# Performance work log

Hardware: AMD Instinct MI355X
Metric: run time of the kernel (lower is better)

## Reference

```python
import jax, jax.numpy as jnp
import numpy as np

B, S, E, H, L = 64, 256, 640, 512, 2  # batch, seq_len, input_size(=embed+sum_depth), rnn_size, num_layers
ZDIM = L * 2 * 2 * H  # ziphidden output dim = num_layers * num_dirs * (h|c) * H = 4096


def setup_inputs() -> dict:
    key = jax.random.key(0)
    ks = jax.random.split(key, 16)
    s = 0.05  # small init scale (~1/sqrt(H)) to avoid gate saturation
    f32 = jnp.float32
    inp = {
        "input": jax.random.normal(ks[0], (B, S, E), f32),
        "eps": jax.random.normal(ks[1], (B, ZDIM), f32),
        # layer 0 (input E), stacked over 2 directions [fwd, rev]
        "w_ih0": jax.random.normal(ks[2], (2, 4 * H, E), f32) * s,
        "w_hh0": jax.random.normal(ks[3], (2, 4 * H, H), f32) * s,
        "b_ih0": jax.random.normal(ks[4], (2, 4 * H), f32) * s,
        "b_hh0": jax.random.normal(ks[5], (2, 4 * H), f32) * s,
        # layer 1 (input 2H from bidirectional layer-0 output)
        "w_ih1": jax.random.normal(ks[6], (2, 4 * H, 2 * H), f32) * s,
        "w_hh1": jax.random.normal(ks[7], (2, 4 * H, H), f32) * s,
        "b_ih1": jax.random.normal(ks[8], (2, 4 * H), f32) * s,
        "b_hh1": jax.random.normal(ks[9], (2, 4 * H), f32) * s,
        # linear heads (layer_dim*2 -> layer_dim*2)
        "W_mu": jax.random.normal(ks[10], (ZDIM, ZDIM), f32) * 0.02,
        "b_mu": jax.random.normal(ks[11], (ZDIM,), f32) * 0.02,
        "W_var": jax.random.normal(ks[12], (ZDIM, ZDIM), f32) * 0.02,
        "b_var": jax.random.normal(ks[13], (ZDIM,), f32) * 0.02,
    }
    return inp


def _lstm_cell(x, h, c, wih, whh, b):
    # gates order i, f, g, o (PyTorch convention)
    g = x @ wih.T + h @ whh.T + b
    i, f, gg, o = jnp.split(g, 4, axis=-1)
    c2 = jax.nn.sigmoid(f) * c + jax.nn.sigmoid(i) * jnp.tanh(gg)
    h2 = jax.nn.sigmoid(o) * jnp.tanh(c2)
    return h2, c2


def reference(input, eps, w_ih0, w_hh0, b_ih0, b_hh0, w_ih1, w_hh1, b_ih1, b_hh1, W_mu, b_mu, W_var, b_var):
    # Module does input.view(seq_len, batch, embed) (a reshape, not transpose) then
    # steps the LSTM one timestep at a time for seq_len-1 steps. Since each call is
    # a length-1 sequence, both directions see the same single step independently.
    x_seq = input.reshape(S, B, E)[: S - 1]
    W_ih, W_hh = [w_ih0, w_ih1], [w_hh0, w_hh1]
    Bias = [b_ih0 + b_hh0, b_ih1 + b_hh1]

    h0 = jnp.zeros((2 * L, B, H), input.dtype)  # [l0f, l0r, l1f, l1r]
    c0 = jnp.zeros((2 * L, B, H), input.dtype)

    def step(carry, x):
        h, c = carry
        hs, cs = [], []
        inp_l = x
        for l in range(L):
            hf, cf = _lstm_cell(inp_l, h[2 * l], c[2 * l], W_ih[l][0], W_hh[l][0], Bias[l][0])
            hr, cr = _lstm_cell(inp_l, h[2 * l + 1], c[2 * l + 1], W_ih[l][1], W_hh[l][1], Bias[l][1])
            hs += [hf, hr]
            cs += [cf, cr]
            inp_l = jnp.concatenate([hf, hr], axis=-1)  # layer output feeds next layer
        return (jnp.stack(hs), jnp.stack(cs)), None

    (hF, cF), _ = jax.lax.scan(step, (h0, c0), x_seq)

    # ziphidden: cat(h, c, dim=2) -> transpose(0,1) -> view(B, -1)
    z = jnp.concatenate([hF, cF], axis=2)            # [2L, B, 2H]
    z = jnp.transpose(z, (1, 0, 2)).reshape(B, -1)   # [B, ZDIM]

    mu = z @ W_mu.T + b_mu
    logvar = z @ W_var.T + b_var
    # reparameterize (training mode) with externally supplied eps
    return mu + eps * jnp.exp(0.5 * logvar)
```

## Files before the change

kernel.cpp:

```cpp
#include <hip/hip_runtime.h>
#include <hip/hip_bf16.h>
#include <cstddef>
#include <cstdint>

#define B     64
#define S     256
#define E     640
#define H     512
#define TSTEPS (S - 1)
#define ZDIM  4096
#define KT    64
#define HS    (B * H)
#define CELL64 8192
#define NBUF  4

#define FSLOT(c, s) (((c) << 7) + ((s) << 2))

typedef __attribute__((ext_vector_type(8)))  __bf16 bf16x8;
typedef __attribute__((ext_vector_type(16))) float  f32x16;
typedef unsigned long long ull;

__device__ __forceinline__ float sigf(float x) { return 1.0f / (1.0f + __expf(-x)); }
__device__ __forceinline__ float tanhfast(float x) { return 1.0f - 2.0f / (__expf(2.0f * x) + 1.0f); }

__device__ __forceinline__ unsigned short f2bf(float f) {
    union { float f; unsigned u; } x; x.f = f;
    unsigned r = x.u + 0x7fffu + ((x.u >> 16) & 1u);
    return (unsigned short)(r >> 16);
}
__device__ __forceinline__ float bf2f(unsigned short u) {
    union { unsigned u; float f; } x; x.u = ((unsigned)u) << 16;
    return x.f;
}
__device__ __forceinline__ unsigned pk2(float a, float b) {
    return (unsigned)f2bf(a) | ((unsigned)f2bf(b) << 16);
}

#define HSTORE64(p, v) __hip_atomic_store((p), (v), __ATOMIC_RELAXED, __HIP_MEMORY_SCOPE_AGENT)
#define HSTORE32(p, v) __hip_atomic_store((p), (v), __ATOMIC_RELAXED, __HIP_MEMORY_SCOPE_AGENT)

__device__ __forceinline__ uint4 cld16(const void* p) {
    uint4 v;
    asm volatile("global_load_dwordx4 %0, %1, off sc0 sc1"
                 : "=v"(v) : "v"(p) : "memory");
    return v;
}
__device__ __forceinline__ unsigned ldf(const unsigned* p) {
    unsigned v;
    asm volatile("global_load_dword %0, %1, off sc0 sc1"
                 : "=v"(v) : "v"(p) : "memory");
    return v;
}
__device__ __forceinline__ void cwait0() {
    asm volatile("s_waitcnt vmcnt(0)" ::: "memory");
    __builtin_amdgcn_sched_barrier(0);
}
__device__ __forceinline__ void vmw16() {
    asm volatile("s_waitcnt vmcnt(16)" ::: "memory");
    __builtin_amdgcn_sched_barrier(0);
}
__device__ __forceinline__ bf16x8 u2b(uint4 u) {
    union { uint4 u; bf16x8 b; } x; x.u = u; return x.b;
}


__global__ __launch_bounds__(256) void conv_x_kernel(
    const float* __restrict__ in, unsigned short* __restrict__ out, int n8)
{
    int i = blockIdx.x * 256 + threadIdx.x;
    if (i >= n8) return;
    const float4* p = (const float4*)(in + (size_t)i * 8);
    float4 a = p[0], b = p[1];
    unsigned short* o = out + (size_t)i * 8;
    o[0] = f2bf(a.x); o[1] = f2bf(a.y); o[2] = f2bf(a.z); o[3] = f2bf(a.w);
    o[4] = f2bf(b.x); o[5] = f2bf(b.y); o[6] = f2bf(b.z); o[7] = f2bf(b.w);
}

__global__ __launch_bounds__(256) void repack_w_kernel(
    const float* __restrict__ in, unsigned short* __restrict__ out, int K)
{
    int kc = K / 8;
    int i = blockIdx.x * 256 + threadIdx.x;
    if (i >= 2 * 2048 * kc) return;
    int k8 = i % kc;
    int n  = (i / kc) & 2047;
    int d  = i / (kc * 2048);
    int srow = (n & 3) * 512 + (n >> 2);
    const float* src = in + ((size_t)d * 2048 + srow) * K + (size_t)k8 * 8;
    unsigned short* dst = out + ((size_t)d * 2048 + n) * K + (size_t)k8 * 8;
    #pragma unroll
    for (int q = 0; q < 8; ++q) dst[q] = f2bf(src[q]);
}

__global__ __launch_bounds__(256) void pack_bias_kernel(
    const float* __restrict__ bih, const float* __restrict__ bhh, float* __restrict__ out)
{
    int i = blockIdx.x * 256 + threadIdx.x;
    if (i >= 4096) return;
    int d = i >> 11, n = i & 2047;
    int s = d * 2048 + (n & 3) * 512 + (n >> 2);
    out[i] = bih[s] + bhh[s];
}

__global__ __launch_bounds__(256) void xproj_kernel(
    const unsigned short* __restrict__ xb,
    const unsigned short* __restrict__ w0p,
    unsigned short* __restrict__ xp)
{
    extern __shared__ __align__(16) char lds[];
    const int tid = threadIdx.x;
    const int l   = tid & 63;
    const int w   = tid >> 6;
    const int wm  = w & 1, wn = w >> 1;
    const int d   = blockIdx.x >> 5;
    const int n0  = (blockIdx.x & 31) * 64;

    for (int idx = tid; idx < 64 * 80; idx += 256) {
        int r = idx / 80, k8 = idx % 80;
        bf16x8 v = *(const bf16x8*)(w0p + ((size_t)d*2048 + n0 + r)*640 + (size_t)k8*8);
        int o = k8*16 + r*16; o -= (o >= 1280) ? 1280 : 0;
        *(bf16x8*)(lds + r*1280 + o) = v;
    }
    __syncthreads();

    const int lrow  = wn * 32 + (l & 31);
    const int khalf = l >> 5;
    const char* ldsrow = lds + (size_t)lrow * 1280;
    const int rot = lrow * 16 + khalf * 16;
    const int t0 = blockIdx.y * 64;
    const int t1 = (t0 + 64 < TSTEPS) ? (t0 + 64) : TSTEPS;

    for (int t = t0; t < t1; ++t) {
        f32x16 a0, a1;
#pragma unroll
        for (int r = 0; r < 16; ++r) { a0[r] = 0.f; a1[r] = 0.f; }
        const unsigned short* Ax = xb + ((size_t)t*B + wm*32 + (l & 31))*E + khalf*8;
#pragma unroll 8
        for (int k0 = 0; k0 < E; k0 += 16) {
            bf16x8 a = *(const bf16x8*)(Ax + k0);
            int o = k0*2 + rot; o -= (o >= 1280) ? 1280 : 0;
            bf16x8 b = *(const bf16x8*)(ldsrow + o);
            if ((k0 >> 4) & 1) a1 = __builtin_amdgcn_mfma_f32_32x32x16_bf16(a, b, a1, 0, 0, 0);
            else               a0 = __builtin_amdgcn_mfma_f32_32x32x16_bf16(a, b, a0, 0, 0, 0);
        }
        size_t base = ((((size_t)t*2 + d)*64 + (n0 >> 5) + wn)*2 + wm)*1024 + (size_t)l*16;
        unsigned short* dst = xp + base;
        uint4 o0, o1;
        o0.x = pk2(a0[0]+a1[0],  a0[1]+a1[1]);
        o0.y = pk2(a0[2]+a1[2],  a0[3]+a1[3]);
        o0.z = pk2(a0[4]+a1[4],  a0[5]+a1[5]);
        o0.w = pk2(a0[6]+a1[6],  a0[7]+a1[7]);
        o1.x = pk2(a0[8]+a1[8],  a0[9]+a1[9]);
        o1.y = pk2(a0[10]+a1[10], a0[11]+a1[11]);
        o1.z = pk2(a0[12]+a1[12], a0[13]+a1[13]);
        o1.w = pk2(a0[14]+a1[14], a0[15]+a1[15]);
        *(uint4*)dst       = o0;
        *(uint4*)(dst + 8) = o1;
    }
}

__device__ __forceinline__ void poll_l0(const unsigned* flags, int d,
                                        unsigned traw, unsigned twar, int l)
{
    const unsigned* pd = flags + FSLOT(d, l & 31);
    const unsigned* pw = flags + FSLOT((l < 32) ? 2 : 3, l & 31);
    for (;;) {
        unsigned a = ldf(pd);
        unsigned b = ldf(pw);
        cwait0();
        if (__all((int)(a >= traw && b >= twar))) break;
        __builtin_amdgcn_s_sleep(1);
    }
}
__device__ __forceinline__ void poll_l1(const unsigned* flags, int d,
                                        unsigned k, int l)
{
    const unsigned* po = flags + FSLOT(2 + d, l & 31);
    const unsigned* pc = flags + FSLOT((l < 32) ? 0 : 1, l & 31);
    const unsigned town = k - 1u;
    for (;;) {
        unsigned a = ldf(po);
        unsigned b = ldf(pc);
        cwait0();
        if (__all((int)(a >= town && b >= k))) break;
        __builtin_amdgcn_s_sleep(1);
    }
}

__device__ __forceinline__ void hcell_c_lds(const void* hp, const char* ldsrow,
    int rotofs, int wrapB, f32x16& a0, f32x16& a1)
{
    uint4 hv[32];
#pragma unroll
    for (int m = 0; m < 32; ++m)
        hv[m] = cld16((const char*)hp + (size_t)m * 1024);
    cwait0();
#pragma unroll
    for (int m = 0; m < 32; ++m) {
        int o = m*32 + rotofs; o -= (o >= wrapB) ? wrapB : 0;
        bf16x8 b = *(const bf16x8*)(ldsrow + o);
        bf16x8 a = u2b(hv[m]);
        if (m & 1) a1 = __builtin_amdgcn_mfma_f32_32x32x16_bf16(a, b, a1, 0, 0, 0);
        else       a0 = __builtin_amdgcn_mfma_f32_32x32x16_bf16(a, b, a0, 0, 0, 0);
    }
}

__device__ __forceinline__ void issue16(uint4* hv, const char* hpB, int mb) {
#pragma unroll
    for (int j = 0; j < 16; ++j)
        hv[j] = cld16(hpB + (size_t)(mb + j) * 1024);
}
__device__ __forceinline__ void consume16_reg(const uint4* hv, const bf16x8* wf,
                                              int mb, f32x16& a0, f32x16& a1)
{
#pragma unroll
    for (int j = 0; j < 16; ++j) {
        const int m = mb + j;
        bf16x8 a = u2b(hv[j]);
        if (m & 1) a1 = __builtin_amdgcn_mfma_f32_32x32x16_bf16(a, wf[m], a1, 0, 0, 0);
        else       a0 = __builtin_amdgcn_mfma_f32_32x32x16_bf16(a, wf[m], a0, 0, 0, 0);
    }
}
__device__ __forceinline__ void consume16_lds(const uint4* hv, const char* ldsrow,
                                              int rotofs, int mb, f32x16& a0, f32x16& a1)
{
#pragma unroll
    for (int j = 0; j < 16; ++j) {
        const int m = mb + j;
        int o = (m*32 + rotofs) & 2047;
        bf16x8 b = *(const bf16x8*)(ldsrow + o);
        bf16x8 a = u2b(hv[j]);
        if (m & 1) a1 = __builtin_amdgcn_mfma_f32_32x32x16_bf16(a, b, a1, 0, 0, 0);
        else       a0 = __builtin_amdgcn_mfma_f32_32x32x16_bf16(a, b, a0, 0, 0, 0);
    }
}

template<bool XADD>
__device__ __forceinline__ void act_store(
    const f32x16& a0, const f32x16& a1, bf16x8 xpa, bf16x8 xpb,
    int unitg, int wm, int l, float* creg, float* hreg, ull* hq_cell)
{
    const int g  = l & 3;
    const int hi = l >> 5;
    union { bf16x8 v; unsigned short s[8]; } ua, ub;
    ua.v = xpa; ub.v = xpb;
    float gi[4], gf[4], gg[4], go[4];
#pragma unroll
    for (int r = 0; r < 16; ++r) {
        float v0 = a0[r] + a1[r];
        if (XADD) v0 += bf2f((r < 8) ? ua.s[r] : ub.s[r - 8]);
        float v1 = __shfl_xor(v0, 1);
        float v2 = __shfl_xor(v0, 2);
        float v3 = __shfl_xor(v0, 3);
        float pv[4] = {v0, v1, v2, v3};
        const int rg = r & 3, q = r >> 2;
        if (g == rg) { gi[q] = pv[rg^0]; gf[q] = pv[rg^1]; gg[q] = pv[rg^2]; go[q] = pv[rg^3]; }
    }
    const int ubase = unitg & ~3;
    ull* dst = hq_cell + wm*4096 + (ubase >> 4)*128 + ((ubase >> 3) & 1)*64
                       + ((ubase >> 2) & 1);
#pragma unroll
    for (int q = 0; q < 4; ++q) {
        int rl = g + 8*q + 4*hi;
        float cold = creg[q];
        float cnew = sigf(gf[q]) * cold + sigf(gi[q]) * tanhfast(gg[q]);
        float hnew = sigf(go[q]) * tanhfast(cnew);
        creg[q] = cnew;
        hreg[q] = hnew;
        unsigned m  = f2bf(hnew);
        unsigned o1 = __shfl_xor(m, 4);
        unsigned d0 = (unitg & 1) ? ((m << 16) | o1) : ((o1 << 16) | m);
        unsigned o2 = __shfl_xor(d0, 8);
        ull q64 = (unitg & 2) ? (((ull)d0 << 32) | (ull)o2) : (((ull)o2 << 32) | (ull)d0);
        if ((l & 12) == 0)
            HSTORE64(dst + rl*2, q64);
    }
}

template<int XPRE>
__global__ __launch_bounds__(256, 1) void persist_kernel(
    const unsigned short* __restrict__ xb,
    const unsigned short* __restrict__ w0p,
    const unsigned short* __restrict__ wh0p,
    const unsigned short* __restrict__ w1p,
    const unsigned short* __restrict__ wh1p,
    const float* __restrict__ b0p,
    const float* __restrict__ b1p,
    const unsigned short* __restrict__ xp,
    unsigned short* __restrict__ hbuf,
    float* __restrict__ cbuf,
    unsigned short* __restrict__ hplain,
    unsigned* __restrict__ flags)
{
    extern __shared__ __align__(16) char lds[];
    const int tid = threadIdx.x;
    const int l   = tid & 63;
    const int w   = tid >> 6;
    const int wm  = w & 1, wn = w >> 1;
    const int bid = blockIdx.x;
    const bool isL1 = bid >= 64;
    const int g2 = bid & 63;
    const int d  = g2 >> 5;
    const int n0 = (g2 & 31) * 64;
    const int myslot = g2 & 31;
    const int lrow  = wn * 32 + (l & 31);
    const int khalf = l >> 5;
    const int HHOFF = 64 * 1280;

    if (!isL1) {
        if (!XPRE) {
            for (int idx = tid; idx < 64 * 80; idx += 256) {
                int r = idx / 80, k8 = idx % 80;
                bf16x8 v = *(const bf16x8*)(w0p + ((size_t)d*2048 + n0 + r)*640 + (size_t)k8*8);
                int o = k8*16 + r*16; o -= (o >= 1280) ? 1280 : 0;
                *(bf16x8*)(lds + r*1280 + o) = v;
            }
        }
        const int hb0 = XPRE ? 0 : HHOFF;
        for (int idx = tid; idx < 64 * 64; idx += 256) {
            int r = idx / 64, k8 = idx % 64;
            bf16x8 v = *(const bf16x8*)(wh0p + ((size_t)d*2048 + n0 + r)*512 + (size_t)k8*8);
            int o = k8*16 + r*16; o -= (o >= 1024) ? 1024 : 0;
            *(bf16x8*)(lds + hb0 + r*1024 + o) = v;
        }
    } else {
        for (int idx = tid; idx < 64 * 128; idx += 256) {
            int r = idx / 128, k8 = idx % 128;
            bf16x8 v = *(const bf16x8*)(w1p + ((size_t)d*2048 + n0 + r)*1024 + (size_t)k8*8);
            int o = k8*16 + r*16; o -= (o >= 2048) ? 2048 : 0;
            *(bf16x8*)(lds + r*2048 + o) = v;
        }
    }
    __syncthreads();

    const float bias = (isL1 ? b1p : b0p)[d*2048 + n0 + lrow];
    const char* ldsrow_ih = lds + (size_t)lrow * (isL1 ? 2048 : 1280);
    const char* ldsrow_hh = lds + (XPRE ? 0 : HHOFF) + (size_t)lrow * 1024;
    const int rot = lrow * 16 + khalf * 16;
    const int unitg = ((n0 + lrow) >> 2);
    const int hoff  = wm*4096 + khalf*64 + (l & 31)*2;
    const int arow  = wm * 32 + (l & 31);
    float creg[4] = {0.f, 0.f, 0.f, 0.f};
    float hreg[4] = {0.f, 0.f, 0.f, 0.f};
    const ull* hb = (const ull*)hbuf;
    ull*       hw = (ull*)hbuf;
    const int mycell = isL1 ? (2 + d) : d;
    unsigned* myflag = flags + FSLOT(mycell, myslot);
    bf16x8 zero8 = {};

    bf16x8 wh[32];
    if (isL1) {
        const unsigned short* whl = wh1p + ((size_t)d*2048 + n0 + lrow)*512 + khalf*8;
#pragma unroll
        for (int m = 0; m < 32; ++m) wh[m] = *(const bf16x8*)(whl + m*16);
    }

    for (int k = 0; k <= TSTEPS; ++k) {
        const int rbuf = k % NBUF, wbuf = (k + 1) % NBUF;
        const size_t rb = (size_t)rbuf * 4 * CELL64;
        const size_t wb = (size_t)wbuf * 4 * CELL64;
        if (!isL1) {
            if (k < TSTEPS) {
                f32x16 a0, a1;
#pragma unroll
                for (int r = 0; r < 16; ++r) { a0[r] = bias; a1[r] = 0.f; }
                bf16x8 xpa = zero8, xpb = zero8;
                if (XPRE) {
                    size_t base = ((((size_t)k*2 + d)*64 + (n0 >> 5) + wn)*2 + wm)*1024
                                  + (size_t)l*16;
                    xpa = *(const bf16x8*)(xp + base);
                    xpb = *(const bf16x8*)(xp + base + 8);
                } else {
                    const unsigned short* Ax = xb + (size_t)k*B*E + (size_t)arow*E + khalf*8;
#pragma unroll 8
                    for (int k0 = 0; k0 < E; k0 += 16) {
                        bf16x8 a = *(const bf16x8*)(Ax + k0);
                        int o = k0*2 + rot; o -= (o >= 1280) ? 1280 : 0;
                        bf16x8 b = *(const bf16x8*)(ldsrow_ih + o);
                        if ((k0 >> 4) & 1) a1 = __builtin_amdgcn_mfma_f32_32x32x16_bf16(a, b, a1, 0, 0, 0);
                        else               a0 = __builtin_amdgcn_mfma_f32_32x32x16_bf16(a, b, a0, 0, 0, 0);
                    }
                }
                if (k >= 1) {
                    if (w == 0)
                        poll_l0(flags, d, (unsigned)k,
                                (k >= 3) ? (unsigned)(k - 3) : 0u, l);
                    __syncthreads();
                }
                hcell_c_lds((const char*)(hb + rb + (size_t)d*CELL64 + hoff),
                            ldsrow_hh, rot, 1024, a0, a1);
                act_store<true>(a0, a1, xpa, xpb, unitg, wm, l, creg, hreg,
                                hw + wb + (size_t)d*CELL64);
                asm volatile("s_waitcnt vmcnt(0)" ::: "memory");
                __syncthreads();
                if (tid == 0) HSTORE32(myflag, (unsigned)(k + 1));
            }
        } else {
            if (k >= 1) {
                f32x16 a0, a1;
#pragma unroll
                for (int r = 0; r < 16; ++r) { a0[r] = bias; a1[r] = 0.f; }
                if (w == 0) poll_l1(flags, d, (unsigned)k, l);
                __syncthreads();
                const char* hpO = (const char*)(hb + rb + (size_t)(2+d)*CELL64 + hoff);
                const char* hp0 = (const char*)(hb + rb + (size_t)0*CELL64 + hoff);
                const char* hp1 = (const char*)(hb + rb + (size_t)1*CELL64 + hoff);
                uint4 hvA[16], hvB[16];
                issue16(hvA, hpO, 0);
                issue16(hvB, hpO, 16);
                vmw16(); consume16_reg(hvA, wh, 0,  a0, a1);
                issue16(hvA, hp0, 0);
                vmw16(); consume16_reg(hvB, wh, 16, a0, a1);
                issue16(hvB, hp0, 16);
                vmw16(); consume16_lds(hvA, ldsrow_ih, rot, 0,  a0, a1);
                issue16(hvA, hp1, 0);
                vmw16(); consume16_lds(hvB, ldsrow_ih, rot, 16, a0, a1);
                issue16(hvB, hp1, 16);
                vmw16(); consume16_lds(hvA, ldsrow_ih, rot + 1024, 0,  a0, a1);
                cwait0(); consume16_lds(hvB, ldsrow_ih, rot + 1024, 16, a0, a1);
                act_store<false>(a0, a1, zero8, zero8, unitg, wm, l, creg, hreg,
                                 hw + wb + (size_t)(2+d)*CELL64);
                asm volatile("s_waitcnt vmcnt(0)" ::: "memory");
                __syncthreads();
                if (tid == 0) HSTORE32(myflag, (unsigned)k);
            }
        }
    }

    {
        float*          cc = cbuf   + (size_t)mycell * HS;
        unsigned short* hh = hplain + (size_t)mycell * HS;
        const int g = l & 3, hi = l >> 5;
#pragma unroll
        for (int q = 0; q < 4; ++q) {
            int row = 32*wm + g + 8*q + 4*hi;
            cc[(size_t)row * 512 + unitg] = creg[q];
            hh[(size_t)row * 512 + unitg] = f2bf(hreg[q]);
        }
    }
}

__global__ __launch_bounds__(256) void head_kernel(
    const unsigned short* __restrict__ hplain,
    const float* __restrict__ cbuf,
    const float* __restrict__ eps,
    const float* __restrict__ Wmu,  const float* __restrict__ bmu,
    const float* __restrict__ Wvar, const float* __restrict__ bvar,
    float* __restrict__ out)
{
    const int tid = threadIdx.x;
    const int b   = tid & 63;
    const int i   = blockIdx.x * 4 + (tid >> 6);

    __shared__ float zs[KT][B + 1];

    float amu = 0.f, alv = 0.f;
    const float* wm = Wmu  + (size_t)i * ZDIM;
    const float* wv = Wvar + (size_t)i * ZDIM;

    for (int k0 = 0; k0 < ZDIM; k0 += KT) {
        __syncthreads();
        for (int idx = tid; idx < (B * KT) / 4; idx += 256) {
            int bb  = idx / (KT / 4);
            int kq4 = (idx % (KT / 4)) * 4;
            int zk  = k0 + kq4;
            int cell = zk >> 10;
            int m    = zk & 1023;
            float4 v;
            if (m < H) {
                const unsigned short* hs = hplain + (size_t)cell * HS + (size_t)bb * H + m;
                v.x = bf2f(hs[0]); v.y = bf2f(hs[1]); v.z = bf2f(hs[2]); v.w = bf2f(hs[3]);
            } else {
                v = *(const float4*)(cbuf + (size_t)cell * HS + (size_t)bb * H + (m - H));
            }
            zs[kq4 + 0][bb] = v.x; zs[kq4 + 1][bb] = v.y;
            zs[kq4 + 2][bb] = v.z; zs[kq4 + 3][bb] = v.w;
        }
        __syncthreads();
        #pragma unroll
        for (int kk = 0; kk < KT; kk += 4) {
            float4 a = *(const float4*)(wm + k0 + kk);
            float4 c = *(const float4*)(wv + k0 + kk);
            float z0 = zs[kk + 0][b], z1 = zs[kk + 1][b];
            float z2 = zs[kk + 2][b], z3 = zs[kk + 3][b];
            amu += a.x * z0 + a.y * z1 + a.z * z2 + a.w * z3;
            alv += c.x * z0 + c.y * z1 + c.z * z2 + c.w * z3;
        }
    }
    float mu = amu + bmu[i];
    float lv = alv + bvar[i];
    out[(size_t)b * ZDIM + i] = mu + eps[(size_t)b * ZDIM + i] * __expf(0.5f * lv);
}

extern "C" void kernel_launch(void* const* d_in, const int* in_sizes, int n_in,
                              void* d_out, int out_size, void* d_ws, size_t ws_size,
                              hipStream_t stream) {
    const float* input = (const float*)d_in[0];
    const float* eps   = (const float*)d_in[1];
    const float* w_ih0 = (const float*)d_in[2];
    const float* w_hh0 = (const float*)d_in[3];
    const float* b_ih0 = (const float*)d_in[4];
    const float* b_hh0 = (const float*)d_in[5];
    const float* w_ih1 = (const float*)d_in[6];
    const float* w_hh1 = (const float*)d_in[7];
    const float* b_ih1 = (const float*)d_in[8];
    const float* b_hh1 = (const float*)d_in[9];
    const float* W_mu  = (const float*)d_in[10];
    const float* b_mu  = (const float*)d_in[11];
    const float* W_var = (const float*)d_in[12];
    const float* b_var = (const float*)d_in[13];
    float* out = (float*)d_out;

    uint8_t* base = (uint8_t*)d_ws;
    size_t off = 0;
    auto alloc = [&](size_t bytes) -> void* {
        void* p = base + off;
        off += (bytes + 255) & ~(size_t)255;
        return p;
    };
    unsigned short* xb   = (unsigned short*)alloc((size_t)TSTEPS * B * E * 2);
    unsigned short* w0p  = (unsigned short*)alloc((size_t)2 * 2048 * E * 2);
    unsigned short* wh0p = (unsigned short*)alloc((size_t)2 * 2048 * H * 2);
    unsigned short* w1p  = (unsigned short*)alloc((size_t)2 * 2048 * 1024 * 2);
    unsigned short* wh1p = (unsigned short*)alloc((size_t)2 * 2048 * H * 2);
    float* b0p = (float*)alloc(2 * 2048 * 4);
    float* b1p = (float*)alloc(2 * 2048 * 4);
    unsigned* flags      = (unsigned*)alloc(2048);
    unsigned short* hbuf = (unsigned short*)alloc((size_t)NBUF * 4 * HS * 2);
    float* cbuf          = (float*)alloc((size_t)4 * HS * 4);
    unsigned short* hplain = (unsigned short*)alloc((size_t)4 * HS * 2);
    unsigned short* xp   = (unsigned short*)alloc((size_t)TSTEPS * 2 * 2048 * B * 2);
    const bool XPRE = (ws_size >= off);

    hipMemsetAsync(flags, 0, 2048 + (size_t)NBUF * 4 * HS * 2, stream);

    conv_x_kernel<<<(TSTEPS * B * E / 8 + 255) / 256, 256, 0, stream>>>(input, xb, TSTEPS * B * E / 8);
    repack_w_kernel<<<(2 * 2048 * (E / 8) + 255) / 256, 256, 0, stream>>>(w_ih0, w0p, E);
    repack_w_kernel<<<(2 * 2048 * (H / 8) + 255) / 256, 256, 0, stream>>>(w_hh0, wh0p, H);
    repack_w_kernel<<<(2 * 2048 * (1024 / 8) + 255) / 256, 256, 0, stream>>>(w_ih1, w1p, 1024);
    repack_w_kernel<<<(2 * 2048 * (H / 8) + 255) / 256, 256, 0, stream>>>(w_hh1, wh1p, H);
    pack_bias_kernel<<<16, 256, 0, stream>>>(b_ih0, b_hh0, b0p);
    pack_bias_kernel<<<16, 256, 0, stream>>>(b_ih1, b_hh1, b1p);

    const size_t lds_persist = 144 * 1024;
    if (XPRE) {
        const size_t lds_xp = 84 * 1024;
        hipFuncSetAttribute((const void*)xproj_kernel,
                            hipFuncAttributeMaxDynamicSharedMemorySize, (int)lds_xp);
        xproj_kernel<<<dim3(64, 4), 256, lds_xp, stream>>>(xb, w0p, xp);
        hipFuncSetAttribute((const void*)persist_kernel<1>,
                            hipFuncAttributeMaxDynamicSharedMemorySize, (int)lds_persist);
        persist_kernel<1><<<128, 256, lds_persist, stream>>>(
            xb, w0p, wh0p, w1p, wh1p, b0p, b1p, xp, hbuf, cbuf, hplain, flags);
    } else {
        hipFuncSetAttribute((const void*)persist_kernel<0>,
                            hipFuncAttributeMaxDynamicSharedMemorySize, (int)lds_persist);
        persist_kernel<0><<<128, 256, lds_persist, stream>>>(
            xb, w0p, wh0p, w1p, wh1p, b0p, b1p, xp, hbuf, cbuf, hplain, flags);
    }

    head_kernel<<<ZDIM / 4, 256, 0, stream>>>(hplain, cbuf, eps, W_mu, b_mu, W_var, b_var, out);
}
```

Before: 2.922 ms.

## Fuse input projection into persistent kernel as producer blocks with flag sync

The separate xproj kernel and the fp32-to-bf16 conversion kernel are removed. The persistent kernel now launches 256 blocks, and the extra 128 blocks compute the layer-0 input projection straight from the fp32 input. After each timestep they publish a per-tile progress flag, and layer-0 recurrent blocks poll that flag before reading the projection, so projection work overlaps the recurrence instead of running before it. This relies on all 256 blocks being co-resident (one per CU at 144KB LDS) and adds polling overhead to every layer-0 step.

```diff
diff --git a/kernel.cpp b/kernel.cpp
--- a/kernel.cpp
+++ b/kernel.cpp
@@ -102,73 +102,23 @@
     out[i] = bih[s] + bhh[s];
 }
 
-__global__ __launch_bounds__(256) void xproj_kernel(
-    const unsigned short* __restrict__ xb,
-    const unsigned short* __restrict__ w0p,
-    unsigned short* __restrict__ xp)
-{
-    extern __shared__ __align__(16) char lds[];
-    const int tid = threadIdx.x;
-    const int l   = tid & 63;
-    const int w   = tid >> 6;
-    const int wm  = w & 1, wn = w >> 1;
-    const int d   = blockIdx.x >> 5;
-    const int n0  = (blockIdx.x & 31) * 64;
-
-    for (int idx = tid; idx < 64 * 80; idx += 256) {
-        int r = idx / 80, k8 = idx % 80;
-        bf16x8 v = *(const bf16x8*)(w0p + ((size_t)d*2048 + n0 + r)*640 + (size_t)k8*8);
-        int o = k8*16 + r*16; o -= (o >= 1280) ? 1280 : 0;
-        *(bf16x8*)(lds + r*1280 + o) = v;
-    }
-    __syncthreads();
-
-    const int lrow  = wn * 32 + (l & 31);
-    const int khalf = l >> 5;
-    const char* ldsrow = lds + (size_t)lrow * 1280;
-    const int rot = lrow * 16 + khalf * 16;
-    const int t0 = blockIdx.y * 64;
-    const int t1 = (t0 + 64 < TSTEPS) ? (t0 + 64) : TSTEPS;
-
-    for (int t = t0; t < t1; ++t) {
-        f32x16 a0, a1;
-#pragma unroll
-        for (int r = 0; r < 16; ++r) { a0[r] = 0.f; a1[r] = 0.f; }
-        const unsigned short* Ax = xb + ((size_t)t*B + wm*32 + (l & 31))*E + khalf*8;
-#pragma unroll 8
-        for (int k0 = 0; k0 < E; k0 += 16) {
-            bf16x8 a = *(const bf16x8*)(Ax + k0);
-            int o = k0*2 + rot; o -= (o >= 1280) ? 1280 : 0;
-            bf16x8 b = *(const bf16x8*)(ldsrow + o);
-            if ((k0 >> 4) & 1) a1 = __builtin_amdgcn_mfma_f32_32x32x16_bf16(a, b, a1, 0, 0, 0);
-            else               a0 = __builtin_amdgcn_mfma_f32_32x32x16_bf16(a, b, a0, 0, 0, 0);
-        }
-        size_t base = ((((size_t)t*2 + d)*64 + (n0 >> 5) + wn)*2 + wm)*1024 + (size_t)l*16;
-        unsigned short* dst = xp + base;
-        uint4 o0, o1;
-        o0.x = pk2(a0[0]+a1[0],  a0[1]+a1[1]);
-        o0.y = pk2(a0[2]+a1[2],  a0[3]+a1[3]);
-        o0.z = pk2(a0[4]+a1[4],  a0[5]+a1[5]);
-        o0.w = pk2(a0[6]+a1[6],  a0[7]+a1[7]);
-        o1.x = pk2(a0[8]+a1[8],  a0[9]+a1[9]);
-        o1.y = pk2(a0[10]+a1[10], a0[11]+a1[11]);
-        o1.z = pk2(a0[12]+a1[12], a0[13]+a1[13]);
-        o1.w = pk2(a0[14]+a1[14], a0[15]+a1[15]);
-        *(uint4*)dst       = o0;
-        *(uint4*)(dst + 8) = o1;
-    }
-}
-
-__device__ __forceinline__ void poll_l0(const unsigned* flags, int d,
-                                        unsigned traw, unsigned twar, int l)
+
+template<int XPRE>
+__device__ __forceinline__ void poll_l0(const unsigned* flags, int d, int tile,
+                                        unsigned traw, unsigned twar,
+                                        unsigned tA, unsigned tB, int l)
 {
     const unsigned* pd = flags + FSLOT(d, l & 31);
     const unsigned* pw = flags + FSLOT((l < 32) ? 2 : 3, l & 31);
+    const unsigned* px = flags + 512 + (((d*32 + tile)*2 + (l & 1)) << 2);
+    const unsigned tx = (l & 1) ? tB : tA;
     for (;;) {
         unsigned a = ldf(pd);
         unsigned b = ldf(pw);
+        unsigned c = XPRE ? ldf(px) : 0xFFFFFFFFu;
         cwait0();
-        if (__all((int)(a >= traw && b >= twar))) break;
+        bool ok = (a >= traw) && (b >= twar) && (l >= 2 || c >= tx);
+        if (__all((int)ok)) break;
         __builtin_amdgcn_s_sleep(1);
     }
 }
@@ -187,17 +137,24 @@
     }
 }
 
-__device__ __forceinline__ void hcell_c_lds(const void* hp, const char* ldsrow,
-    int rotofs, int wrapB, f32x16& a0, f32x16& a1)
-{
-    uint4 hv[32];
+template<int XPRE>
+__device__ __forceinline__ void hcell_l0(const void* hp, const void* xpp,
+    const char* ldsrow, int rotofs, f32x16& a0, f32x16& a1,
+    bf16x8& xpa, bf16x8& xpb)
+{
+    uint4 hv[32], xv0, xv1;
+    if (XPRE) {
+        xv0 = cld16(xpp);
+        xv1 = cld16((const char*)xpp + 16);
+    }
 #pragma unroll
     for (int m = 0; m < 32; ++m)
         hv[m] = cld16((const char*)hp + (size_t)m * 1024);
     cwait0();
+    if (XPRE) { xpa = u2b(xv0); xpb = u2b(xv1); }
 #pragma unroll
     for (int m = 0; m < 32; ++m) {
-        int o = m*32 + rotofs; o -= (o >= wrapB) ? wrapB : 0;
+        int o = (m*32 + rotofs) & 1023;
         bf16x8 b = *(const bf16x8*)(ldsrow + o);
         bf16x8 a = u2b(hv[m]);
         if (m & 1) a1 = __builtin_amdgcn_mfma_f32_32x32x16_bf16(a, b, a1, 0, 0, 0);
@@ -279,6 +236,7 @@
 
 template<int XPRE>
 __global__ __launch_bounds__(256, 1) void persist_kernel(
+    const float* __restrict__ xin,
     const unsigned short* __restrict__ xb,
     const unsigned short* __restrict__ w0p,
     const unsigned short* __restrict__ wh0p,
@@ -286,7 +244,7 @@
     const unsigned short* __restrict__ wh1p,
     const float* __restrict__ b0p,
     const float* __restrict__ b1p,
-    const unsigned short* __restrict__ xp,
+    unsigned short* __restrict__ xp,
     unsigned short* __restrict__ hbuf,
     float* __restrict__ cbuf,
     unsigned short* __restrict__ hplain,
@@ -298,14 +256,71 @@
     const int w   = tid >> 6;
     const int wm  = w & 1, wn = w >> 1;
     const int bid = blockIdx.x;
+    const int lrow  = wn * 32 + (l & 31);
+    const int khalf = l >> 5;
+    const int HHOFF = 64 * 1280;
+
+    if (XPRE && bid >= 128) {
+        const int bid2 = bid - 128;
+        const int dd   = bid2 >> 6;
+        const int tile = (bid2 >> 1) & 31;
+        const int half = bid2 & 1;
+        const int n0p  = tile * 64;
+        for (int idx = tid; idx < 64 * 80; idx += 256) {
+            int r = idx / 80, k8 = idx % 80;
+            bf16x8 v = *(const bf16x8*)(w0p + ((size_t)dd*2048 + n0p + r)*640 + (size_t)k8*8);
+            int o = k8*16 + r*16; o -= (o >= 1280) ? 1280 : 0;
+            *(bf16x8*)(lds + r*1280 + o) = v;
+        }
+        __syncthreads();
+        const char* ldsrow = lds + (size_t)lrow * 1280;
+        const int rot = lrow * 16 + khalf * 16;
+        const int t0 = half * 128, t1 = half ? TSTEPS : 128;
+        unsigned* pxf = flags + 512 + (((dd*32 + tile)*2 + half) << 2);
+        for (int t = t0; t < t1; ++t) {
+            f32x16 a0, a1;
+#pragma unroll
+            for (int r = 0; r < 16; ++r) { a0[r] = 0.f; a1[r] = 0.f; }
+            const float* Af = xin + ((size_t)t*B + wm*32 + (l & 31))*E + khalf*8;
+#pragma unroll 8
+            for (int k0 = 0; k0 < E; k0 += 16) {
+                float4 f0 = *(const float4*)(Af + k0);
+                float4 f1 = *(const float4*)(Af + k0 + 4);
+                uint4 ua;
+                ua.x = pk2(f0.x, f0.y); ua.y = pk2(f0.z, f0.w);
+                ua.z = pk2(f1.x, f1.y); ua.w = pk2(f1.z, f1.w);
+                bf16x8 a = u2b(ua);
+                int o = k0*2 + rot; o -= (o >= 1280) ? 1280 : 0;
+                bf16x8 b = *(const bf16x8*)(ldsrow + o);
+                if ((k0 >> 4) & 1) a1 = __builtin_amdgcn_mfma_f32_32x32x16_bf16(a, b, a1, 0, 0, 0);
+                else               a0 = __builtin_amdgcn_mfma_f32_32x32x16_bf16(a, b, a0, 0, 0, 0);
+            }
+            size_t base = ((((size_t)t*2 + dd)*64 + tile*2 + wn)*2 + wm)*1024 + (size_t)l*16;
+            ull* dst = (ull*)(xp + base);
+            union { uint4 v; ull q[2]; } c0, c1;
+            c0.v.x = pk2(a0[0]+a1[0],  a0[1]+a1[1]);
+            c0.v.y = pk2(a0[2]+a1[2],  a0[3]+a1[3]);
+            c0.v.z = pk2(a0[4]+a1[4],  a0[5]+a1[5]);
+            c0.v.w = pk2(a0[6]+a1[6],  a0[7]+a1[7]);
+            c1.v.x = pk2(a0[8]+a1[8],  a0[9]+a1[9]);
+            c1.v.y = pk2(a0[10]+a1[10], a0[11]+a1[11]);
+            c1.v.z = pk2(a0[12]+a1[12], a0[13]+a1[13]);
+            c1.v.w = pk2(a0[14]+a1[14], a0[15]+a1[15]);
+            HSTORE64(dst + 0, c0.q[0]); HSTORE64(dst + 1, c0.q[1]);
+            HSTORE64(dst + 2, c1.q[0]); HSTORE64(dst + 3, c1.q[1]);
+            asm volatile("s_waitcnt vmcnt(0)" ::: "memory");
+            __syncthreads();
+            if (tid == 0) HSTORE32(pxf, (unsigned)(t - t0 + 1));
+        }
+        return;
+    }
+
     const bool isL1 = bid >= 64;
     const int g2 = bid & 63;
     const int d  = g2 >> 5;
     const int n0 = (g2 & 31) * 64;
     const int myslot = g2 & 31;
-    const int lrow  = wn * 32 + (l & 31);
-    const int khalf = l >> 5;
-    const int HHOFF = 64 * 1280;
+    const int tile   = g2 & 31;
 
     if (!isL1) {
         if (!XPRE) {
@@ -365,12 +380,7 @@
 #pragma unroll
                 for (int r = 0; r < 16; ++r) { a0[r] = bias; a1[r] = 0.f; }
                 bf16x8 xpa = zero8, xpb = zero8;
-                if (XPRE) {
-                    size_t base = ((((size_t)k*2 + d)*64 + (n0 >> 5) + wn)*2 + wm)*1024
-                                  + (size_t)l*16;
-                    xpa = *(const bf16x8*)(xp + base);
-                    xpb = *(const bf16x8*)(xp + base + 8);
-                } else {
+                if (!XPRE) {
                     const unsigned short* Ax = xb + (size_t)k*B*E + (size_t)arow*E + khalf*8;
 #pragma unroll 8
                     for (int k0 = 0; k0 < E; k0 += 16) {
@@ -381,14 +391,20 @@
                         else               a0 = __builtin_amdgcn_mfma_f32_32x32x16_bf16(a, b, a0, 0, 0, 0);
                     }
                 }
-                if (k >= 1) {
-                    if (w == 0)
-                        poll_l0(flags, d, (unsigned)k,
-                                (k >= 3) ? (unsigned)(k - 3) : 0u, l);
-                    __syncthreads();
+                {
+                    unsigned tA = XPRE ? ((k < 128) ? (unsigned)(k + 1) : 128u) : 0u;
+                    unsigned tB = XPRE ? ((k < 128) ? 0u : (unsigned)(k - 127)) : 0u;
+                    unsigned traw = (k >= 1) ? (unsigned)k : 0u;
+                    unsigned twar = (k >= 3) ? (unsigned)(k - 3) : 0u;
+                    if (XPRE || k >= 1) {
+                        if (w == 0) poll_l0<XPRE>(flags, d, tile, traw, twar, tA, tB, l);
+                        __syncthreads();
+                    }
                 }
-                hcell_c_lds((const char*)(hb + rb + (size_t)d*CELL64 + hoff),
-                            ldsrow_hh, rot, 1024, a0, a1);
+                const char* xpp = (const char*)xp +
+                    (((((size_t)k*2 + d)*64 + tile*2 + wn)*2 + wm)*1024 + (size_t)l*16) * 2;
+                hcell_l0<XPRE>((const char*)(hb + rb + (size_t)d*CELL64 + hoff), xpp,
+                               ldsrow_hh, rot, a0, a1, xpa, xpb);
                 act_store<true>(a0, a1, xpa, xpb, unitg, wm, l, creg, hreg,
                                 hw + wb + (size_t)d*CELL64);
                 asm volatile("s_waitcnt vmcnt(0)" ::: "memory");
@@ -525,16 +541,15 @@
     unsigned short* wh1p = (unsigned short*)alloc((size_t)2 * 2048 * H * 2);
     float* b0p = (float*)alloc(2 * 2048 * 4);
     float* b1p = (float*)alloc(2 * 2048 * 4);
-    unsigned* flags      = (unsigned*)alloc(2048);
+    unsigned* flags      = (unsigned*)alloc(4096);
     unsigned short* hbuf = (unsigned short*)alloc((size_t)NBUF * 4 * HS * 2);
     float* cbuf          = (float*)alloc((size_t)4 * HS * 4);
     unsigned short* hplain = (unsigned short*)alloc((size_t)4 * HS * 2);
     unsigned short* xp   = (unsigned short*)alloc((size_t)TSTEPS * 2 * 2048 * B * 2);
     const bool XPRE = (ws_size >= off);
 
-    hipMemsetAsync(flags, 0, 2048 + (size_t)NBUF * 4 * HS * 2, stream);
-
-    conv_x_kernel<<<(TSTEPS * B * E / 8 + 255) / 256, 256, 0, stream>>>(input, xb, TSTEPS * B * E / 8);
+    hipMemsetAsync(flags, 0, 4096 + (size_t)NBUF * 4 * HS * 2, stream);
+
     repack_w_kernel<<<(2 * 2048 * (E / 8) + 255) / 256, 256, 0, stream>>>(w_ih0, w0p, E);
     repack_w_kernel<<<(2 * 2048 * (H / 8) + 255) / 256, 256, 0, stream>>>(w_hh0, wh0p, H);
     repack_w_kernel<<<(2 * 2048 * (1024 / 8) + 255) / 256, 256, 0, stream>>>(w_ih1, w1p, 1024);
@@ -544,19 +559,17 @@
 
     const size_t lds_persist = 144 * 1024;
     if (XPRE) {
-        const size_t lds_xp = 84 * 1024;
-        hipFuncSetAttribute((const void*)xproj_kernel,
-                            hipFuncAttributeMaxDynamicSharedMemorySize, (int)lds_xp);
-        xproj_kernel<<<dim3(64, 4), 256, lds_xp, stream>>>(xb, w0p, xp);
         hipFuncSetAttribute((const void*)persist_kernel<1>,
                             hipFuncAttributeMaxDynamicSharedMemorySize, (int)lds_persist);
-        persist_kernel<1><<<128, 256, lds_persist, stream>>>(
-            xb, w0p, wh0p, w1p, wh1p, b0p, b1p, xp, hbuf, cbuf, hplain, flags);
+        persist_kernel<1><<<256, 256, lds_persist, stream>>>(
+            input, xb, w0p, wh0p, w1p, wh1p, b0p, b1p, xp, hbuf, cbuf, hplain, flags);
     } else {
+        conv_x_kernel<<<(TSTEPS * B * E / 8 + 255) / 256, 256, 0, stream>>>(
+            input, xb, TSTEPS * B * E / 8);
         hipFuncSetAttribute((const void*)persist_kernel<0>,
                             hipFuncAttributeMaxDynamicSharedMemorySize, (int)lds_persist);
         persist_kernel<0><<<128, 256, lds_persist, stream>>>(
-            xb, w0p, wh0p, w1p, wh1p, b0p, b1p, xp, hbuf, cbuf, hplain, flags);
+            input, xb, w0p, wh0p, w1p, wh1p, b0p, b1p, xp, hbuf, cbuf, hplain, flags);
     }
 
     head_kernel<<<ZDIM / 4, 256, 0, stream>>>(hplain, cbuf, eps, W_mu, b_mu, W_var, b_var, out);
```

New measurement: 2.763 ms. -5.4%, faster.
